# Performance work log

Hardware: AMD Instinct MI355X
Metric: run time of the kernel (lower is better)

Reference implementation:

```python
import jax, jax.numpy as jnp
import numpy as np

B, N, D = 4096, 128, 256


def setup_inputs() -> dict:
    key = jax.random.key(0)
    ks = jax.random.split(key, 6)
    return {
        "label": jax.random.normal(ks[0], (B, N, D), dtype=jnp.float32),
        "adj_in": jax.random.uniform(ks[1], (N, N), dtype=jnp.float32),
        "adj_out": jax.random.uniform(ks[2], (N, N), dtype=jnp.float32),
        "edge_bias": jnp.zeros((N, D), dtype=jnp.float32),
        "gate_weight": jax.random.normal(ks[3], (D, 1), dtype=jnp.float32) * (6.0 / (D + 1)) ** 0.5,
        "bias_gate": jnp.zeros((N, 1), dtype=jnp.float32),
        "out_edge_bias": jnp.zeros((N, D), dtype=jnp.float32),
        "out_gate_weight": jax.random.normal(ks[4], (D, 1), dtype=jnp.float32) * (6.0 / (D + 1)) ** 0.5,
        "out_bias_gate": jnp.zeros((N, 1), dtype=jnp.float32),
        "loop_gate": jax.random.normal(ks[5], (D, 1), dtype=jnp.float32) * (6.0 / (D + 1)) ** 0.5,
    }


def reference(label, adj_in, adj_out, edge_bias, gate_weight, bias_gate,
              out_edge_bias, out_gate_weight, out_bias_gate, loop_gate):
    h = label  # [B, N, D]
    # origin_adj is a constant buffer in the original module (detached numpy)
    origin = jax.lax.stop_gradient(jnp.where(adj_in <= 0, adj_in, 1.0))

    # in-arc branch: masked dense adjacency matmul + bias + scalar gate
    h_in = jnp.einsum('mn,bnd->bmd', origin * adj_in, h)            # [B, N, D]
    in_gate = jnp.einsum('bnd,do->bno', h, gate_weight) + bias_gate  # [B, N, 1]
    msg_in = (h_in + edge_bias) * jax.nn.sigmoid(in_gate)

    # out-arc branch: transposed mask times out adjacency
    h_out = jnp.einsum('mn,bnd->bmd', origin.T * adj_out, h)
    out_gate = jnp.einsum('bnd,do->bno', h, out_gate_weight) + out_bias_gate
    msg_out = (h_out + out_edge_bias) * jax.nn.sigmoid(out_gate)

    # self-loop branch
    lp_gate = jnp.einsum('bnd,do->bno', h, loop_gate)
    msg_loop = h * jax.nn.sigmoid(lp_gate)

    # dropout p=0.0 -> identity
    return jax.nn.relu(msg_in + msg_out + msg_loop)
```

## Files before the change

kernel.cpp:

```cpp
#include <hip/hip_runtime.h>
#include <hip/hip_bf16.h>

#define NN 128
#define ND 256

typedef __attribute__((ext_vector_type(8))) short short8v;
typedef __attribute__((ext_vector_type(4))) short short4v;
typedef __attribute__((ext_vector_type(4))) float floatx4;

__device__ __forceinline__ unsigned short f2bf(float x){
  unsigned u = __float_as_uint(x);
  u += 0x7FFF + ((u >> 16) & 1);
  return (unsigned short)(u >> 16);
}
__device__ __forceinline__ float bf2f(unsigned short h){
  return __uint_as_float(((unsigned)h) << 16);
}

__global__ void prep_A(const float* __restrict__ adj_in, const float* __restrict__ adj_out,
                       const float* __restrict__ gw, const float* __restrict__ ogw,
                       const float* __restrict__ lw, unsigned short* __restrict__ Abf){
  int idx = blockIdx.x * 256 + threadIdx.x;
  if (idx < 32768){
    int m = idx >> 7, n = idx & 127;
    float v;
    if (m < NN){
      float a = adj_in[m * NN + n];
      v = (a <= 0.f) ? a * a : a;
    } else {
      int mm = m - NN;
      float t = adj_in[n * NN + mm];
      float o = (t <= 0.f) ? t : 1.f;
      v = o * adj_out[mm * NN + n];
    }
    Abf[idx] = f2bf(v);
  } else if (idx < 32768 + 4096){
    int t   = idx - 32768;
    int j   = t & 7, m16 = (t >> 3) & 15, g = (t >> 7) & 3, kc = t >> 9;
    int d   = kc * 32 + 8 * g + j;
    float v = (m16 == 0) ? gw[d] : (m16 == 1) ? ogw[d] : (m16 == 2) ? lw[d] : 0.f;
    Abf[idx] = f2bf(v);
  }
}

__global__ __launch_bounds__(512, 4) void gcn_main(
    const float* __restrict__ H, const unsigned short* __restrict__ Abf,
    const float* __restrict__ eb,  const float* __restrict__ bg,
    const float* __restrict__ oeb, const float* __restrict__ obg,
    float* __restrict__ Out)
{
  __shared__ __align__(16) unsigned short Ht[ND * NN];
  __shared__ float sigS[3 * NN];

  const int tid  = threadIdx.x;
  const int wave = tid >> 6;
  const int lane = tid & 63;
  const int g    = lane >> 4;
  const int m16  = lane & 15;
  const int b    = blockIdx.x;
  const float* Hb = H   + (size_t)b * NN * ND;
  float*       Ob = Out + (size_t)b * NN * ND;
  const unsigned short* WgT = Abf + 32768;

  const int G    = 4 * wave + g;
  const int n0   = 4 * G;
  const int arow = 16 * wave + m16;

  floatx4 gacc = {0.f, 0.f, 0.f, 0.f};
  #pragma unroll
  for (int s = 0; s < 4; ++s){
    #pragma unroll
    for (int t = 0; t < 2; ++t){
      const int k0 = 64 * s + 32 * t;
      const floatx4 f0 = *(const floatx4*)(Hb + (size_t)arow * ND + k0 + 8 * g);
      const floatx4 f1 = *(const floatx4*)(Hb + (size_t)arow * ND + k0 + 8 * g + 4);
      const short8v wv = *(const short8v*)&WgT[(((k0 >> 5) * 4 + g) * 16 + m16) * 8];
      short8v af;
      af[0] = (short)f2bf(f0[0]); af[1] = (short)f2bf(f0[1]);
      af[2] = (short)f2bf(f0[2]); af[3] = (short)f2bf(f0[3]);
      af[4] = (short)f2bf(f1[0]); af[5] = (short)f2bf(f1[1]);
      af[6] = (short)f2bf(f1[2]); af[7] = (short)f2bf(f1[3]);
      gacc = __builtin_amdgcn_mfma_f32_16x16x32_bf16(af, wv, gacc, 0, 0, 0);
    }
    const int d0 = 64 * s + 4 * m16;
    floatx4 rr[4];
    #pragma unroll
    for (int ro = 0; ro < 4; ++ro)
      rr[ro] = *(const floatx4*)(Hb + (size_t)(n0 + ro) * ND + d0);
    #pragma unroll
    for (int j = 0; j < 4; ++j){
      const int d = d0 + j;
      short4v pv;
      pv[0] = (short)f2bf(rr[0][j]);
      pv[1] = (short)f2bf(rr[1][j]);
      pv[2] = (short)f2bf(rr[2][j]);
      pv[3] = (short)f2bf(rr[3][j]);
      *(short4v*)&Ht[d * NN + (n0 ^ (((d >> 1) & 7) << 3))] = pv;
    }
  }
  if (m16 < 3){
    #pragma unroll
    for (int r = 0; r < 4; ++r){
      const int n = 16 * wave + 4 * g + r;
      float x = gacc[r];
      if (m16 == 0)      x += bg[n];
      else if (m16 == 1) x += obg[n];
      sigS[m16 * NN + n] = 1.f / (1.f + __expf(-x));
    }
  }
  __syncthreads();

  const float si = sigS[arow];
  const float so = sigS[NN + arow];
  const float sl = sigS[2 * NN + arow];

  const floatx4 zz = {0.f, 0.f, 0.f, 0.f};
  #pragma unroll
  for (int pass = 0; pass < 2; ++pass){
    const int dbase = 128 * pass;
    floatx4 acc1[8], acc2[8];
    #pragma unroll
    for (int i = 0; i < 8; ++i){ acc1[i] = zz; acc2[i] = zz; }

    #pragma unroll
    for (int k0 = 0; k0 < 128; k0 += 32){
      const int kk = k0 + 8 * g;
      const short8v av1 = *(const short8v*)&Abf[ arow        * 128 + kk];
      const short8v av2 = *(const short8v*)&Abf[(128 + arow) * 128 + kk];
      #pragma unroll
      for (int df = 0; df < 8; ++df){
        const int d = dbase + 16 * df + m16;
        const short8v hv = *(const short8v*)&Ht[d * NN + (kk ^ (((d >> 1) & 7) << 3))];
        acc1[df] = __builtin_amdgcn_mfma_f32_16x16x32_bf16(hv, av1, acc1[df], 0, 0, 0);
        acc2[df] = __builtin_amdgcn_mfma_f32_16x16x32_bf16(hv, av2, acc2[df], 0, 0, 0);
      }
    }

    #pragma unroll
    for (int df = 0; df < 8; ++df){
      const int dcol = dbase + 16 * df + 4 * g;
      const floatx4 ebv  = *(const floatx4*)(eb  + arow * ND + dcol);
      const floatx4 oebv = *(const floatx4*)(oeb + arow * ND + dcol);
      float hl[4];
      #pragma unroll
      for (int r = 0; r < 4; ++r){
        const int d = dcol + r;
        hl[r] = bf2f(Ht[d * NN + (arow ^ (((d >> 1) & 7) << 3))]);
      }
      floatx4 o;
      #pragma unroll
      for (int r = 0; r < 4; ++r){
        const float v = (acc1[df][r] + ebv[r]) * si
                      + (acc2[df][r] + oebv[r]) * so
                      + hl[r] * sl;
        o[r] = fmaxf(v, 0.f);
      }
      __builtin_nontemporal_store(o, (floatx4*)(Ob + (size_t)arow * ND + dcol));
    }
  }
}

extern "C" void kernel_launch(void* const* d_in, const int* in_sizes, int n_in,
                              void* d_out, int out_size, void* d_ws, size_t ws_size,
                              hipStream_t stream){
  const float* H    = (const float*)d_in[0];
  const float* ain  = (const float*)d_in[1];
  const float* aout = (const float*)d_in[2];
  const float* eb   = (const float*)d_in[3];
  const float* gwp  = (const float*)d_in[4];
  const float* bgp  = (const float*)d_in[5];
  const float* oebp = (const float*)d_in[6];
  const float* ogwp = (const float*)d_in[7];
  const float* obgp = (const float*)d_in[8];
  const float* lwp  = (const float*)d_in[9];
  unsigned short* Abf = (unsigned short*)d_ws;

  prep_A<<<144, 256, 0, stream>>>(ain, aout, gwp, ogwp, lwp, Abf);
  gcn_main<<<4096, 512, 0, stream>>>(H, Abf, eb, bgp, oebp, obgp, (float*)d_out);
}
```

Baseline: 373.8 us.

## Double-buffer LDS halves across two batches per block to overlap loads with MFMA

Each block now processes two batch elements and splits the feature dimension into 128-wide halves. The next half is staged in registers while the current half runs its MFMAs, then written to a second LDS buffer, so global loads overlap tensor math. The gates for both batches are computed up front. The change also switches to packed bf16x2 conversion and raises wave priority around the MFMA loop. The aim is to hide global load latency in this memory-bound kernel. In exchange it halves the grid, adds more syncs and staging registers, and keeps LDS use per block unchanged.

```diff
diff --git a/kernel.cpp b/kernel.cpp
--- a/kernel.cpp
+++ b/kernel.cpp
@@ -7,6 +7,8 @@
 typedef __attribute__((ext_vector_type(8))) short short8v;
 typedef __attribute__((ext_vector_type(4))) short short4v;
 typedef __attribute__((ext_vector_type(4))) float floatx4;
+typedef __attribute__((ext_vector_type(2))) unsigned int uint2v;
+typedef __attribute__((ext_vector_type(4))) unsigned int uint4v;
 
 __device__ __forceinline__ unsigned short f2bf(float x){
   unsigned u = __float_as_uint(x);
@@ -15,6 +17,13 @@
 }
 __device__ __forceinline__ float bf2f(unsigned short h){
   return __uint_as_float(((unsigned)h) << 16);
+}
+__device__ __forceinline__ unsigned pk2(float a, float b){
+  float2 t; t.x = a; t.y = b;
+  __hip_bfloat162 h = __float22bfloat162_rn(t);
+  unsigned r;
+  __builtin_memcpy(&r, &h, 4);
+  return r;
 }
 
 __global__ void prep_A(const float* __restrict__ adj_in, const float* __restrict__ adj_out,
@@ -49,113 +58,135 @@
     const float* __restrict__ oeb, const float* __restrict__ obg,
     float* __restrict__ Out)
 {
-  __shared__ __align__(16) unsigned short Ht[ND * NN];
-  __shared__ float sigS[3 * NN];
+  __shared__ __align__(16) unsigned short Ht[2][128 * NN];
+  __shared__ float sigS[2][3 * NN];
 
   const int tid  = threadIdx.x;
   const int wave = tid >> 6;
   const int lane = tid & 63;
   const int g    = lane >> 4;
   const int m16  = lane & 15;
-  const int b    = blockIdx.x;
-  const float* Hb = H   + (size_t)b * NN * ND;
-  float*       Ob = Out + (size_t)b * NN * ND;
+  const int n0   = 4 * (4 * wave + g);
+  const int arow = 16 * wave + m16;
+
+  const size_t base0 = (size_t)(2 * blockIdx.x) * NN * ND;
+  const float* Hb[2] = { H + base0, H + base0 + (size_t)NN * ND };
+  float*       Ob[2] = { Out + base0, Out + base0 + (size_t)NN * ND };
   const unsigned short* WgT = Abf + 32768;
 
-  const int G    = 4 * wave + g;
-  const int n0   = 4 * G;
-  const int arow = 16 * wave + m16;
-
-  floatx4 gacc = {0.f, 0.f, 0.f, 0.f};
+  floatx4 ga[2];
+  ga[0] = (floatx4){0.f,0.f,0.f,0.f};
+  ga[1] = (floatx4){0.f,0.f,0.f,0.f};
   #pragma unroll
-  for (int s = 0; s < 4; ++s){
-    #pragma unroll
-    for (int t = 0; t < 2; ++t){
-      const int k0 = 64 * s + 32 * t;
-      const floatx4 f0 = *(const floatx4*)(Hb + (size_t)arow * ND + k0 + 8 * g);
-      const floatx4 f1 = *(const floatx4*)(Hb + (size_t)arow * ND + k0 + 8 * g + 4);
-      const short8v wv = *(const short8v*)&WgT[(((k0 >> 5) * 4 + g) * 16 + m16) * 8];
+  for (int c = 0; c < 8; ++c){
+    const int k0 = 32 * c;
+    const short8v wv = *(const short8v*)&WgT[((c * 4 + g) * 16 + m16) * 8];
+    #pragma unroll
+    for (int q = 0; q < 2; ++q){
+      const floatx4 f0 = *(const floatx4*)(Hb[q] + (size_t)arow * ND + k0 + 8 * g);
+      const floatx4 f1 = *(const floatx4*)(Hb[q] + (size_t)arow * ND + k0 + 8 * g + 4);
+      uint4v au;
+      au[0] = pk2(f0[0], f0[1]); au[1] = pk2(f0[2], f0[3]);
+      au[2] = pk2(f1[0], f1[1]); au[3] = pk2(f1[2], f1[3]);
       short8v af;
-      af[0] = (short)f2bf(f0[0]); af[1] = (short)f2bf(f0[1]);
-      af[2] = (short)f2bf(f0[2]); af[3] = (short)f2bf(f0[3]);
-      af[4] = (short)f2bf(f1[0]); af[5] = (short)f2bf(f1[1]);
-      af[6] = (short)f2bf(f1[2]); af[7] = (short)f2bf(f1[3]);
-      gacc = __builtin_amdgcn_mfma_f32_16x16x32_bf16(af, wv, gacc, 0, 0, 0);
-    }
-    const int d0 = 64 * s + 4 * m16;
-    floatx4 rr[4];
-    #pragma unroll
-    for (int ro = 0; ro < 4; ++ro)
-      rr[ro] = *(const floatx4*)(Hb + (size_t)(n0 + ro) * ND + d0);
-    #pragma unroll
-    for (int j = 0; j < 4; ++j){
-      const int d = d0 + j;
-      short4v pv;
-      pv[0] = (short)f2bf(rr[0][j]);
-      pv[1] = (short)f2bf(rr[1][j]);
-      pv[2] = (short)f2bf(rr[2][j]);
-      pv[3] = (short)f2bf(rr[3][j]);
-      *(short4v*)&Ht[d * NN + (n0 ^ (((d >> 1) & 7) << 3))] = pv;
+      __builtin_memcpy(&af, &au, 16);
+      ga[q] = __builtin_amdgcn_mfma_f32_16x16x32_bf16(af, wv, ga[q], 0, 0, 0);
     }
   }
   if (m16 < 3){
     #pragma unroll
-    for (int r = 0; r < 4; ++r){
-      const int n = 16 * wave + 4 * g + r;
-      float x = gacc[r];
-      if (m16 == 0)      x += bg[n];
-      else if (m16 == 1) x += obg[n];
-      sigS[m16 * NN + n] = 1.f / (1.f + __expf(-x));
-    }
-  }
-  __syncthreads();
-
-  const float si = sigS[arow];
-  const float so = sigS[NN + arow];
-  const float sl = sigS[2 * NN + arow];
-
-  const floatx4 zz = {0.f, 0.f, 0.f, 0.f};
-  #pragma unroll
-  for (int pass = 0; pass < 2; ++pass){
-    const int dbase = 128 * pass;
-    floatx4 acc1[8], acc2[8];
-    #pragma unroll
-    for (int i = 0; i < 8; ++i){ acc1[i] = zz; acc2[i] = zz; }
-
+    for (int q = 0; q < 2; ++q){
+      #pragma unroll
+      for (int r = 0; r < 4; ++r){
+        const int n = 16 * wave + 4 * g + r;
+        float x = ga[q][r];
+        if (m16 == 0)      x += bg[n];
+        else if (m16 == 1) x += obg[n];
+        sigS[q][m16 * NN + n] = 1.f / (1.f + __expf(-x));
+      }
+    }
+  }
+
+  floatx4 st[2][4];
+  auto stage_load = [&](const float* Hx, int h){
+    #pragma unroll
+    for (int dq = 0; dq < 2; ++dq){
+      const int dglob = 128 * h + 64 * dq + 4 * m16;
+      #pragma unroll
+      for (int ro = 0; ro < 4; ++ro)
+        st[dq][ro] = *(const floatx4*)(Hx + (size_t)(n0 + ro) * ND + dglob);
+    }
+  };
+  auto stage_write = [&](int buf){
+    #pragma unroll
+    for (int dq = 0; dq < 2; ++dq){
+      const int d0 = 64 * dq + 4 * m16;
+      #pragma unroll
+      for (int j = 0; j < 4; ++j){
+        const int d = d0 + j;
+        uint2v pv;
+        pv[0] = pk2(st[dq][0][j], st[dq][1][j]);
+        pv[1] = pk2(st[dq][2][j], st[dq][3][j]);
+        *(uint2v*)&Ht[buf][d * NN + (n0 ^ (((d >> 1) & 7) << 3))] = pv;
+      }
+    }
+  };
+  auto compute_half = [&](int q, int h, int buf, int half){
+    const float si = sigS[q][arow];
+    const float so = sigS[q][NN + arow];
+    const float sl = sigS[q][2 * NN + arow];
+    floatx4 acc1[4], acc2[4];
+    #pragma unroll
+    for (int i = 0; i < 4; ++i){
+      acc1[i] = (floatx4){0.f,0.f,0.f,0.f};
+      acc2[i] = (floatx4){0.f,0.f,0.f,0.f};
+    }
+    __builtin_amdgcn_s_setprio(1);
     #pragma unroll
     for (int k0 = 0; k0 < 128; k0 += 32){
       const int kk = k0 + 8 * g;
       const short8v av1 = *(const short8v*)&Abf[ arow        * 128 + kk];
       const short8v av2 = *(const short8v*)&Abf[(128 + arow) * 128 + kk];
       #pragma unroll
-      for (int df = 0; df < 8; ++df){
-        const int d = dbase + 16 * df + m16;
-        const short8v hv = *(const short8v*)&Ht[d * NN + (kk ^ (((d >> 1) & 7) << 3))];
-        acc1[df] = __builtin_amdgcn_mfma_f32_16x16x32_bf16(hv, av1, acc1[df], 0, 0, 0);
-        acc2[df] = __builtin_amdgcn_mfma_f32_16x16x32_bf16(hv, av2, acc2[df], 0, 0, 0);
-      }
-    }
-
-    #pragma unroll
-    for (int df = 0; df < 8; ++df){
-      const int dcol = dbase + 16 * df + 4 * g;
-      const floatx4 ebv  = *(const floatx4*)(eb  + arow * ND + dcol);
-      const floatx4 oebv = *(const floatx4*)(oeb + arow * ND + dcol);
-      float hl[4];
+      for (int df2 = 0; df2 < 4; ++df2){
+        const int d = 16 * (4 * half + df2) + m16;
+        const short8v hv = *(const short8v*)&Ht[buf][d * NN + (kk ^ (((d >> 1) & 7) << 3))];
+        acc1[df2] = __builtin_amdgcn_mfma_f32_16x16x32_bf16(hv, av1, acc1[df2], 0, 0, 0);
+        acc2[df2] = __builtin_amdgcn_mfma_f32_16x16x32_bf16(hv, av2, acc2[df2], 0, 0, 0);
+      }
+    }
+    __builtin_amdgcn_s_setprio(0);
+    #pragma unroll
+    for (int df2 = 0; df2 < 4; ++df2){
+      const int dloc  = 16 * (4 * half + df2) + 4 * g;
+      const int dglob = 128 * h + dloc;
+      const floatx4 ebv  = *(const floatx4*)(eb  + arow * ND + dglob);
+      const floatx4 oebv = *(const floatx4*)(oeb + arow * ND + dglob);
+      floatx4 o;
       #pragma unroll
       for (int r = 0; r < 4; ++r){
-        const int d = dcol + r;
-        hl[r] = bf2f(Ht[d * NN + (arow ^ (((d >> 1) & 7) << 3))]);
-      }
-      floatx4 o;
-      #pragma unroll
-      for (int r = 0; r < 4; ++r){
-        const float v = (acc1[df][r] + ebv[r]) * si
-                      + (acc2[df][r] + oebv[r]) * so
-                      + hl[r] * sl;
+        const int d = dloc + r;
+        const float hl = bf2f(Ht[buf][d * NN + (arow ^ (((d >> 1) & 7) << 3))]);
+        const float v = (acc1[df2][r] + ebv[r]) * si
+                      + (acc2[df2][r] + oebv[r]) * so
+                      + hl * sl;
         o[r] = fmaxf(v, 0.f);
       }
-      __builtin_nontemporal_store(o, (floatx4*)(Ob + (size_t)arow * ND + dcol));
+      __builtin_nontemporal_store(o, (floatx4*)(Ob[q] + (size_t)arow * ND + dglob));
+    }
+  };
+
+  stage_load(Hb[0], 0);
+  stage_write(0);
+  __syncthreads();
+  #pragma unroll
+  for (int ph = 0; ph < 4; ++ph){
+    if (ph < 3) stage_load(Hb[(ph + 1) & 1], (ph + 1) >> 1);
+    compute_half(ph & 1, ph >> 1, ph & 1, 0);
+    compute_half(ph & 1, ph >> 1, ph & 1, 1);
+    if (ph < 3){
+      stage_write((ph + 1) & 1);
+      __syncthreads();
     }
   }
 }
@@ -176,5 +207,5 @@
   unsigned short* Abf = (unsigned short*)d_ws;
 
   prep_A<<<144, 256, 0, stream>>>(ain, aout, gwp, ogwp, lwp, Abf);
-  gcn_main<<<4096, 512, 0, stream>>>(H, Abf, eb, bgp, oebp, obgp, (float*)d_out);
-}
+  gcn_main<<<2048, 512, 0, stream>>>(H, Abf, eb, bgp, oebp, obgp, (float*)d_out);
+}
```

Measured after the change: 513.6 us. +37.4%, slower.
